# Kernel tuning notes

Measured on AMD Instinct MI355X. Metric: run time of the kernel, lower is better.

Reference implementation:

```python
import jax, jax.numpy as jnp
import numpy as np


def setup_inputs() -> dict:
    key = jax.random.key(0)
    ks = jax.random.split(key, 7)
    B, T, D, H, C = 256, 512, 128, 512, 10
    s_ih = 1.0 / np.sqrt(H)
    return {
        "X": jax.random.normal(ks[0], (B, T, D), dtype=jnp.float32),
        "W_ih": jax.random.normal(ks[1], (4 * H, D), dtype=jnp.float32) * s_ih,
        "W_hh": jax.random.normal(ks[2], (4 * H, H), dtype=jnp.float32) * s_ih,
        "b_ih": jax.random.normal(ks[3], (4 * H,), dtype=jnp.float32) * s_ih,
        "b_hh": jax.random.normal(ks[4], (4 * H,), dtype=jnp.float32) * s_ih,
        "W_lin": jax.random.normal(ks[5], (C, H), dtype=jnp.float32) * s_ih,
        "b_lin": jax.random.normal(ks[6], (C,), dtype=jnp.float32) * s_ih,
    }


def _lstm_mean_h(X, W_ih, W_hh, b_ih, b_hh):
    B, T, D = X.shape
    H = W_hh.shape[1]
    # Input projections for all timesteps at once: [T, B, 4H]
    x_proj = jnp.einsum("btd,kd->tbk", X, W_ih) + b_ih + b_hh

    def step(carry, xp):
        h, c = carry
        gates = xp + h @ W_hh.T  # [B, 4H]
        i, f, g, o = jnp.split(gates, 4, axis=-1)  # PyTorch i,f,g,o order
        i = jax.nn.sigmoid(i)
        f = jax.nn.sigmoid(f)
        g = jnp.tanh(g)
        o = jax.nn.sigmoid(o)
        c = f * c + i * g
        h = o * jnp.tanh(c)
        return (h, c), h

    h0 = jnp.zeros((B, H), dtype=X.dtype)
    (_, _), hs = jax.lax.scan(step, (h0, h0), x_proj)  # hs: [T, B, H]
    return jnp.mean(hs, axis=0)  # == sum(h_t)/T


def reference(X, W_ih, W_hh, b_ih, b_hh, W_lin, b_lin):
    states = _lstm_mean_h(X, W_ih, W_hh, b_ih, b_hh)  # [B, H]
    logits = states @ W_lin.T + b_lin  # [B, num_classes]
    return logits
```

## Files before the change

### kernel.cpp

```cpp
#include <hip/hip_runtime.h>
#include <stdint.h>


#define T_STEPS 512
#define BATCH   256
#define DIM     128
#define HID     512
#define NGRP    16
#define BT      16

typedef _Float16 half8 __attribute__((ext_vector_type(8)));
typedef _Float16 half4 __attribute__((ext_vector_type(4)));
typedef float    f32x4 __attribute__((ext_vector_type(4)));
typedef unsigned u32x4 __attribute__((ext_vector_type(4)));

#define SLOT_HALFS (BATCH * HID)
#define FLG_OFF    (2 * SLOT_HALFS * 2)
#define WS_NEEDED  (FLG_OFF + NGRP * 8 * 128)

__device__ __forceinline__ half8 cvt8(f32x4 a, f32x4 b) {
  half8 r;
  r[0]=(_Float16)a[0]; r[1]=(_Float16)a[1]; r[2]=(_Float16)a[2]; r[3]=(_Float16)a[3];
  r[4]=(_Float16)b[0]; r[5]=(_Float16)b[1]; r[6]=(_Float16)b[2]; r[7]=(_Float16)b[3];
  return r;
}
__device__ __forceinline__ half8 load8_cvt(const float* p) {
  const f32x4* q = (const f32x4*)p;
  return cvt8(q[0], q[1]);
}
__device__ __forceinline__ float fsig(float x) {
  return __builtin_amdgcn_rcpf(1.f + __expf(-x));
}
__device__ __forceinline__ float ftanh(float x) {
  return 1.f - 2.f * __builtin_amdgcn_rcpf(1.f + __expf(2.f * x));
}

union h4u { unsigned long long u; half4 h; };
union c16 { unsigned long long u2[2]; u32x4 v; };

__global__ __launch_bounds__(256, 1) void lstm_persistent(
    const float* __restrict__ X,   const float* __restrict__ Wih,
    const float* __restrict__ Whh, const float* __restrict__ bih,
    const float* __restrict__ bhh, const float* __restrict__ Wlin,
    float* __restrict__ out, _Float16* __restrict__ hbuf,
    unsigned* __restrict__ flg)
{
  __shared__ unsigned hsh[4096];

  const int tid  = threadIdx.x;
  const int w    = tid >> 6;
  const int lane = tid & 63;
  const int col  = lane & 15;
  const int q    = lane >> 4;
  const int bid  = blockIdx.x;
  const int g    = bid & 15;
  const int blk  = bid >> 4;
  const int J    = blk * 64 + w * 16;
  const int b_my = g * BT + col;

  half8 whh[16][4];
  half8 wih[4][4];
  #pragma unroll
  for (int kc = 0; kc < 16; ++kc)
    #pragma unroll
    for (int mt = 0; mt < 4; ++mt) {
      const int row = mt * HID + J + col;
      whh[kc][mt] = load8_cvt(Whh + (size_t)row * HID + kc * 32 + q * 8);
    }
  #pragma unroll
  for (int xc = 0; xc < 4; ++xc)
    #pragma unroll
    for (int mt = 0; mt < 4; ++mt) {
      const int row = mt * HID + J + col;
      wih[xc][mt] = load8_cvt(Wih + (size_t)row * DIM + xc * 32 + q * 8);
    }

  float bias[4][4], c_st[4], hsum[4];
  #pragma unroll
  for (int mt = 0; mt < 4; ++mt)
    #pragma unroll
    for (int r = 0; r < 4; ++r) {
      const int row = mt * HID + J + q * 4 + r;
      bias[mt][r] = bih[row] + bhh[row];
    }
  #pragma unroll
  for (int r = 0; r < 4; ++r) { c_st[r] = 0.f; hsum[r] = 0.f; }

  unsigned* gflg = flg + g * 8 * 32;
  const float* Xb = X + (size_t)b_my * T_STEPS * DIM;

  f32x4 xr0[8], xr1[8];
  #pragma unroll
  for (int xc = 0; xc < 4; ++xc) {
    const f32x4* p = (const f32x4*)(Xb + xc * 32 + q * 8);
    xr0[2 * xc] = p[0]; xr0[2 * xc + 1] = p[1];
  }
  f32x4 acc[4];
  #pragma unroll
  for (int mt = 0; mt < 4; ++mt) acc[mt] = (f32x4){0.f, 0.f, 0.f, 0.f};
  #pragma unroll
  for (int xc = 0; xc < 4; ++xc) {
    half8 xb = cvt8(xr0[2 * xc], xr0[2 * xc + 1]);
    #pragma unroll
    for (int mt = 0; mt < 4; ++mt)
      acc[mt] = __builtin_amdgcn_mfma_f32_16x16x32_f16(wih[xc][mt], xb, acc[mt], 0, 0, 0);
  }
  #pragma unroll
  for (int xc = 0; xc < 4; ++xc) {
    const f32x4* p1 = (const f32x4*)(Xb + (size_t)1 * DIM + xc * 32 + q * 8);
    const f32x4* p2 = (const f32x4*)(Xb + (size_t)2 * DIM + xc * 32 + q * 8);
    xr1[2 * xc] = p1[0]; xr1[2 * xc + 1] = p1[1];
    xr0[2 * xc] = p2[0]; xr0[2 * xc + 1] = p2[1];
  }

  for (int t = 0; t < T_STEPS; ++t) {
    if (t > 0) {
      {
        const int fl = lane & 7;
        for (;;) {
          unsigned v = __hip_atomic_load(gflg + fl * 32, __ATOMIC_RELAXED,
                                         __HIP_MEMORY_SCOPE_AGENT);
          if (fl == blk) v = 0xFFFFFFFFu;
          if (__all((int)(v >= (unsigned)t))) break;
        }
      }
      __builtin_amdgcn_sched_barrier(0);

      unsigned long long lo[4], hi[4];
      {
        const unsigned long long* base = (const unsigned long long*)
            (hbuf + (size_t)(t & 1) * SLOT_HALFS + (size_t)b_my * HID);
        #pragma unroll
        for (int i = 0; i < 4; ++i) {
          const int kc = w * 4 + i;
          lo[i] = __hip_atomic_load(base + kc * 8 + q * 2,     __ATOMIC_RELAXED, __HIP_MEMORY_SCOPE_AGENT);
          hi[i] = __hip_atomic_load(base + kc * 8 + q * 2 + 1, __ATOMIC_RELAXED, __HIP_MEMORY_SCOPE_AGENT);
        }
      }
      #pragma unroll
      for (int i = 0; i < 4; ++i) {
        const int kc = w * 4 + i;
        c16 u; u.u2[0] = lo[i]; u.u2[1] = hi[i];
        *(u32x4*)(hsh + kc * 256 + col * 16 + q * 4) = u.v;
      }
      __syncthreads();

      {
        const int tn = (t + 2 < T_STEPS) ? (t + 2) : (T_STEPS - 1);
        const float* xp = Xb + (size_t)tn * DIM + q * 8;
        f32x4* dst = (t & 1) ? xr1 : xr0;
        #pragma unroll
        for (int xc = 0; xc < 4; ++xc) {
          const f32x4* src = (const f32x4*)(xp + xc * 32);
          dst[2 * xc]     = src[0];
          dst[2 * xc + 1] = src[1];
        }
      }

      #pragma unroll
      for (int kc = 0; kc < 16; ++kc) {
        const half8 hb = *(const half8*)(hsh + kc * 256 + col * 16 + q * 4);
        #pragma unroll
        for (int mt = 0; mt < 4; ++mt)
          acc[mt] = __builtin_amdgcn_mfma_f32_16x16x32_f16(whh[kc][mt], hb, acc[mt], 0, 0, 0);
      }
    }

    h4u hv;
    #pragma unroll
    for (int r = 0; r < 4; ++r) {
      const float ig = fsig(acc[0][r] + bias[0][r]);
      const float fg = fsig(acc[1][r] + bias[1][r]);
      const float gg = ftanh(acc[2][r] + bias[2][r]);
      const float og = fsig(acc[3][r] + bias[3][r]);
      const float cc = fg * c_st[r] + ig * gg;
      c_st[r] = cc;
      const float h = og * ftanh(cc);
      hsum[r] += h;
      hv.h[r] = (_Float16)h;
    }

    if (t + 1 < T_STEPS) {
      unsigned long long* hw =
          (unsigned long long*)(hbuf + (size_t)((t + 1) & 1) * SLOT_HALFS
                                + (size_t)b_my * HID + J + q * 4);
      __hip_atomic_store(hw, hv.u, __ATOMIC_RELAXED, __HIP_MEMORY_SCOPE_AGENT);

      __syncthreads();
      if (tid == 0)
        __hip_atomic_store(gflg + blk * 32, (unsigned)(t + 1),
                           __ATOMIC_RELAXED, __HIP_MEMORY_SCOPE_AGENT);

      #pragma unroll
      for (int mt = 0; mt < 4; ++mt) acc[mt] = (f32x4){0.f, 0.f, 0.f, 0.f};
      const f32x4* xbuf = ((t + 1) & 1) ? xr1 : xr0;
      #pragma unroll
      for (int xc = 0; xc < 4; ++xc) {
        half8 xb = cvt8(xbuf[2 * xc], xbuf[2 * xc + 1]);
        #pragma unroll
        for (int mt = 0; mt < 4; ++mt)
          acc[mt] = __builtin_amdgcn_mfma_f32_16x16x32_f16(wih[xc][mt], xb, acc[mt], 0, 0, 0);
      }
    }
  }

  const float inv = 1.0f / (float)T_STEPS;
  float m[4];
  #pragma unroll
  for (int r = 0; r < 4; ++r) m[r] = hsum[r] * inv;
  #pragma unroll
  for (int cls = 0; cls < 10; ++cls) {
    f32x4 wl = *(const f32x4*)(Wlin + (size_t)cls * HID + J + q * 4);
    float p = m[0] * wl[0] + m[1] * wl[1] + m[2] * wl[2] + m[3] * wl[3];
    p += __shfl_xor(p, 16, 64);
    p += __shfl_xor(p, 32, 64);
    if (q == 0) atomicAdd(out + b_my * 10 + cls, p);
  }
}

__global__ void init_out(const float* __restrict__ blin, float* __restrict__ out) {
  const int i = blockIdx.x * blockDim.x + threadIdx.x;
  if (i < BATCH * 10) out[i] = blin[i % 10];
}

extern "C" void kernel_launch(void* const* d_in, const int* in_sizes, int n_in,
                              void* d_out, int out_size, void* d_ws, size_t ws_size,
                              hipStream_t stream) {
  const float* X    = (const float*)d_in[0];
  const float* Wih  = (const float*)d_in[1];
  const float* Whh  = (const float*)d_in[2];
  const float* bih  = (const float*)d_in[3];
  const float* bhh  = (const float*)d_in[4];
  const float* Wlin = (const float*)d_in[5];
  const float* blin = (const float*)d_in[6];
  float* out = (float*)d_out;

  if (ws_size < (size_t)WS_NEEDED) return;

  _Float16* hbuf = (_Float16*)d_ws;
  unsigned* flg  = (unsigned*)((char*)d_ws + FLG_OFF);

  hipMemsetAsync((char*)d_ws + FLG_OFF, 0, NGRP * 8 * 128, stream);
  init_out<<<10, 256, 0, stream>>>(blin, out);
  lstm_persistent<<<128, 256, 0, stream>>>(X, Wih, Whh, bih, bhh, Wlin, out,
                                           hbuf, flg);
}
```

Baseline: 2.832 ms.

## Replace per-block flag barrier with sentinel-valued data polling over a four-slot ring

Drops the per-group flag counters. Consumers now spin directly on the hidden-state data, which is held in a 4-deep ring buffer pre-filled with a sentinel bit pattern. Each producer rewrites its slot two steps ahead as a sentinel and publishes h without a block-wide syncthreads or a separate flag store. The first poll is issued speculatively right after publishing, and the shared-memory tile is double-buffered to avoid a second barrier. The aim is to remove the flag round-trip and barrier latency on the serial recurrence critical path. The cost is correctness risk: a real fp16 value could match the sentinel, and the scheme relies on relaxed-ordering assumptions. It also memsets a larger workspace on every call.

```diff
diff --git a/kernel.cpp b/kernel.cpp
--- a/kernel.cpp
+++ b/kernel.cpp
@@ -8,6 +8,7 @@
 #define HID     512
 #define NGRP    16
 #define BT      16
+#define RBUF    4
 
 typedef _Float16 half8 __attribute__((ext_vector_type(8)));
 typedef _Float16 half4 __attribute__((ext_vector_type(4)));
@@ -15,8 +16,9 @@
 typedef unsigned u32x4 __attribute__((ext_vector_type(4)));
 
 #define SLOT_HALFS (BATCH * HID)
-#define FLG_OFF    (2 * SLOT_HALFS * 2)
-#define WS_NEEDED  (FLG_OFF + NGRP * 8 * 128)
+#define SLOT_U64   (SLOT_HALFS / 4)
+#define WS_NEEDED  (RBUF * SLOT_HALFS * 2)
+#define SENT       0x7F7F7F7F7F7F7F7FULL
 
 __device__ __forceinline__ half8 cvt8(f32x4 a, f32x4 b) {
   half8 r;
@@ -42,10 +44,9 @@
     const float* __restrict__ X,   const float* __restrict__ Wih,
     const float* __restrict__ Whh, const float* __restrict__ bih,
     const float* __restrict__ bhh, const float* __restrict__ Wlin,
-    float* __restrict__ out, _Float16* __restrict__ hbuf,
-    unsigned* __restrict__ flg)
+    float* __restrict__ out, _Float16* __restrict__ hbuf)
 {
-  __shared__ unsigned hsh[4096];
+  __shared__ unsigned hsh[2][4096];
 
   const int tid  = threadIdx.x;
   const int w    = tid >> 6;
@@ -86,8 +87,10 @@
   #pragma unroll
   for (int r = 0; r < 4; ++r) { c_st[r] = 0.f; hsum[r] = 0.f; }
 
-  unsigned* gflg = flg + g * 8 * 32;
   const float* Xb = X + (size_t)b_my * T_STEPS * DIM;
+  unsigned long long* h64 = (unsigned long long*)hbuf;
+  const size_t pub_u64 = ((size_t)b_my * HID + J + q * 4) >> 2;
+  const size_t con_u64 = (((size_t)b_my * HID) >> 2) + q * 2;
 
   f32x4 xr0[8], xr1[8];
   #pragma unroll
@@ -113,56 +116,46 @@
     xr0[2 * xc] = p2[0]; xr0[2 * xc + 1] = p2[1];
   }
 
+  unsigned long long lo[4], hi[4];
+  #pragma unroll
+  for (int i = 0; i < 4; ++i) { lo[i] = SENT; hi[i] = SENT; }
+
   for (int t = 0; t < T_STEPS; ++t) {
+    __hip_atomic_store(h64 + (size_t)((t + 2) & 3) * SLOT_U64 + pub_u64,
+                       (unsigned long long)SENT, __ATOMIC_RELAXED,
+                       __HIP_MEMORY_SCOPE_AGENT);
+
     if (t > 0) {
-      {
-        const int fl = lane & 7;
-        for (;;) {
-          unsigned v = __hip_atomic_load(gflg + fl * 32, __ATOMIC_RELAXED,
-                                         __HIP_MEMORY_SCOPE_AGENT);
-          if (fl == blk) v = 0xFFFFFFFFu;
-          if (__all((int)(v >= (unsigned)t))) break;
-        }
-      }
-      __builtin_amdgcn_sched_barrier(0);
-
-      unsigned long long lo[4], hi[4];
-      {
-        const unsigned long long* base = (const unsigned long long*)
-            (hbuf + (size_t)(t & 1) * SLOT_HALFS + (size_t)b_my * HID);
+      const unsigned long long* hp = h64 + (size_t)(t & 3) * SLOT_U64 + con_u64;
+      for (;;) {
+        int ok = 1;
+        #pragma unroll
+        for (int i = 0; i < 4; ++i)
+          ok &= (int)(lo[i] != SENT) & (int)(hi[i] != SENT);
+        if (__all(ok)) break;
         #pragma unroll
         for (int i = 0; i < 4; ++i) {
           const int kc = w * 4 + i;
-          lo[i] = __hip_atomic_load(base + kc * 8 + q * 2,     __ATOMIC_RELAXED, __HIP_MEMORY_SCOPE_AGENT);
-          hi[i] = __hip_atomic_load(base + kc * 8 + q * 2 + 1, __ATOMIC_RELAXED, __HIP_MEMORY_SCOPE_AGENT);
+          lo[i] = __hip_atomic_load(hp + kc * 8,     __ATOMIC_RELAXED, __HIP_MEMORY_SCOPE_AGENT);
+          hi[i] = __hip_atomic_load(hp + kc * 8 + 1, __ATOMIC_RELAXED, __HIP_MEMORY_SCOPE_AGENT);
         }
       }
+      __builtin_amdgcn_sched_barrier(0);
+
       #pragma unroll
       for (int i = 0; i < 4; ++i) {
         const int kc = w * 4 + i;
         c16 u; u.u2[0] = lo[i]; u.u2[1] = hi[i];
-        *(u32x4*)(hsh + kc * 256 + col * 16 + q * 4) = u.v;
+        *(u32x4*)(&hsh[t & 1][kc * 256 + q * 64 + col * 4]) = u.v;
       }
       __syncthreads();
 
-      {
-        const int tn = (t + 2 < T_STEPS) ? (t + 2) : (T_STEPS - 1);
-        const float* xp = Xb + (size_t)tn * DIM + q * 8;
-        f32x4* dst = (t & 1) ? xr1 : xr0;
-        #pragma unroll
-        for (int xc = 0; xc < 4; ++xc) {
-          const f32x4* src = (const f32x4*)(xp + xc * 32);
-          dst[2 * xc]     = src[0];
-          dst[2 * xc + 1] = src[1];
-        }
-      }
-
       #pragma unroll
       for (int kc = 0; kc < 16; ++kc) {
-        const half8 hb = *(const half8*)(hsh + kc * 256 + col * 16 + q * 4);
+        const half8 hbv = *(const half8*)(&hsh[t & 1][kc * 256 + q * 64 + col * 4]);
         #pragma unroll
         for (int mt = 0; mt < 4; ++mt)
-          acc[mt] = __builtin_amdgcn_mfma_f32_16x16x32_f16(whh[kc][mt], hb, acc[mt], 0, 0, 0);
+          acc[mt] = __builtin_amdgcn_mfma_f32_16x16x32_f16(whh[kc][mt], hbv, acc[mt], 0, 0, 0);
       }
     }
 
@@ -181,15 +174,33 @@
     }
 
     if (t + 1 < T_STEPS) {
-      unsigned long long* hw =
-          (unsigned long long*)(hbuf + (size_t)((t + 1) & 1) * SLOT_HALFS
-                                + (size_t)b_my * HID + J + q * 4);
-      __hip_atomic_store(hw, hv.u, __ATOMIC_RELAXED, __HIP_MEMORY_SCOPE_AGENT);
-
-      __syncthreads();
-      if (tid == 0)
-        __hip_atomic_store(gflg + blk * 32, (unsigned)(t + 1),
-                           __ATOMIC_RELAXED, __HIP_MEMORY_SCOPE_AGENT);
+      asm volatile("s_waitcnt vmcnt(0)" ::: "memory");
+
+      __hip_atomic_store(h64 + (size_t)((t + 1) & 3) * SLOT_U64 + pub_u64,
+                         hv.u, __ATOMIC_RELAXED, __HIP_MEMORY_SCOPE_AGENT);
+
+      {
+        const unsigned long long* hp2 =
+            h64 + (size_t)((t + 1) & 3) * SLOT_U64 + con_u64;
+        #pragma unroll
+        for (int i = 0; i < 4; ++i) {
+          const int kc = w * 4 + i;
+          lo[i] = __hip_atomic_load(hp2 + kc * 8,     __ATOMIC_RELAXED, __HIP_MEMORY_SCOPE_AGENT);
+          hi[i] = __hip_atomic_load(hp2 + kc * 8 + 1, __ATOMIC_RELAXED, __HIP_MEMORY_SCOPE_AGENT);
+        }
+      }
+
+      {
+        const int tn = (t + 2 < T_STEPS) ? (t + 2) : (T_STEPS - 1);
+        const float* xp = Xb + (size_t)tn * DIM + q * 8;
+        f32x4* dst = (t & 1) ? xr1 : xr0;
+        #pragma unroll
+        for (int xc = 0; xc < 4; ++xc) {
+          const f32x4* src = (const f32x4*)(xp + xc * 32);
+          dst[2 * xc]     = src[0];
+          dst[2 * xc + 1] = src[1];
+        }
+      }
 
       #pragma unroll
       for (int mt = 0; mt < 4; ++mt) acc[mt] = (f32x4){0.f, 0.f, 0.f, 0.f};
@@ -238,10 +249,9 @@
   if (ws_size < (size_t)WS_NEEDED) return;
 
   _Float16* hbuf = (_Float16*)d_ws;
-  unsigned* flg  = (unsigned*)((char*)d_ws + FLG_OFF);
-
-  hipMemsetAsync((char*)d_ws + FLG_OFF, 0, NGRP * 8 * 128, stream);
+
+  hipMemsetAsync(d_ws, 0x7F, WS_NEEDED, stream);
   init_out<<<10, 256, 0, stream>>>(blin, out);
   lstm_persistent<<<128, 256, 0, stream>>>(X, Wih, Whh, bih, bhh, Wlin, out,
-                                           hbuf, flg);
-}
+                                           hbuf);
+}
```

Result: slower. 3.735 ms (+31.9%).

## Replace per-block step flags with per-wave flags and ring-buffer hidden state

Applied to the files above, without the earlier changes.

Each wave now publishes its slice of h and raises its own readiness flag after waiting only for its own stores. This removes the block-wide barrier before signalling. Consumers poll just the 8 producer waves whose columns they read. To stay safe without that barrier, h moves to a 4-slot global ring and the LDS staging buffer is double-buffered, so faster waves cannot overwrite data still being read. The X prefetch for step t+2 moves after the publish so it stays off the critical path, at the cost of more flag memory and polling traffic.

```diff
diff --git a/kernel.cpp b/kernel.cpp
--- a/kernel.cpp
+++ b/kernel.cpp
@@ -8,6 +8,7 @@
 #define HID     512
 #define NGRP    16
 #define BT      16
+#define RBUF    4
 
 typedef _Float16 half8 __attribute__((ext_vector_type(8)));
 typedef _Float16 half4 __attribute__((ext_vector_type(4)));
@@ -15,8 +16,9 @@
 typedef unsigned u32x4 __attribute__((ext_vector_type(4)));
 
 #define SLOT_HALFS (BATCH * HID)
-#define FLG_OFF    (2 * SLOT_HALFS * 2)
-#define WS_NEEDED  (FLG_OFF + NGRP * 8 * 128)
+#define SLOT_U64   (SLOT_HALFS / 4)
+#define FLG_OFF    (RBUF * SLOT_HALFS * 2)
+#define WS_NEEDED  (FLG_OFF + NGRP * 32 * 128)
 
 __device__ __forceinline__ half8 cvt8(f32x4 a, f32x4 b) {
   half8 r;
@@ -45,7 +47,7 @@
     float* __restrict__ out, _Float16* __restrict__ hbuf,
     unsigned* __restrict__ flg)
 {
-  __shared__ unsigned hsh[4096];
+  __shared__ unsigned hsh[2][4096];
 
   const int tid  = threadIdx.x;
   const int w    = tid >> 6;
@@ -56,6 +58,7 @@
   const int g    = bid & 15;
   const int blk  = bid >> 4;
   const int J    = blk * 64 + w * 16;
+  const int wid  = blk * 4 + w;
   const int b_my = g * BT + col;
 
   half8 whh[16][4];
@@ -86,8 +89,15 @@
   #pragma unroll
   for (int r = 0; r < 4; ++r) { c_st[r] = 0.f; hsum[r] = 0.f; }
 
-  unsigned* gflg = flg + g * 8 * 32;
+  unsigned* gflg = flg + (size_t)g * 32 * 32;
   const float* Xb = X + (size_t)b_my * T_STEPS * DIM;
+  unsigned long long* h64 = (unsigned long long*)hbuf;
+  const size_t pub_u64 = ((size_t)b_my * HID + J + q * 4) >> 2;
+  const size_t con_u64 = ((size_t)b_my * HID) >> 2;
+
+  const int  pw   = 8 * w + (lane & 7);
+  const bool self = (pw == wid);
+  unsigned* pollp = gflg + (size_t)pw * 32;
 
   f32x4 xr0[8], xr1[8];
   #pragma unroll
@@ -115,21 +125,18 @@
 
   for (int t = 0; t < T_STEPS; ++t) {
     if (t > 0) {
-      {
-        const int fl = lane & 7;
-        for (;;) {
-          unsigned v = __hip_atomic_load(gflg + fl * 32, __ATOMIC_RELAXED,
-                                         __HIP_MEMORY_SCOPE_AGENT);
-          if (fl == blk) v = 0xFFFFFFFFu;
-          if (__all((int)(v >= (unsigned)t))) break;
-        }
+      for (;;) {
+        unsigned v = __hip_atomic_load(pollp, __ATOMIC_RELAXED,
+                                       __HIP_MEMORY_SCOPE_AGENT);
+        if (self) v = 0xFFFFFFFFu;
+        if (__all((int)(v >= (unsigned)t))) break;
       }
       __builtin_amdgcn_sched_barrier(0);
 
       unsigned long long lo[4], hi[4];
       {
-        const unsigned long long* base = (const unsigned long long*)
-            (hbuf + (size_t)(t & 1) * SLOT_HALFS + (size_t)b_my * HID);
+        const unsigned long long* base =
+            h64 + (size_t)(t & 3) * SLOT_U64 + con_u64;
         #pragma unroll
         for (int i = 0; i < 4; ++i) {
           const int kc = w * 4 + i;
@@ -141,28 +148,16 @@
       for (int i = 0; i < 4; ++i) {
         const int kc = w * 4 + i;
         c16 u; u.u2[0] = lo[i]; u.u2[1] = hi[i];
-        *(u32x4*)(hsh + kc * 256 + col * 16 + q * 4) = u.v;
+        *(u32x4*)(&hsh[t & 1][kc * 256 + q * 64 + col * 4]) = u.v;
       }
       __syncthreads();
 
-      {
-        const int tn = (t + 2 < T_STEPS) ? (t + 2) : (T_STEPS - 1);
-        const float* xp = Xb + (size_t)tn * DIM + q * 8;
-        f32x4* dst = (t & 1) ? xr1 : xr0;
-        #pragma unroll
-        for (int xc = 0; xc < 4; ++xc) {
-          const f32x4* src = (const f32x4*)(xp + xc * 32);
-          dst[2 * xc]     = src[0];
-          dst[2 * xc + 1] = src[1];
-        }
-      }
-
       #pragma unroll
       for (int kc = 0; kc < 16; ++kc) {
-        const half8 hb = *(const half8*)(hsh + kc * 256 + col * 16 + q * 4);
+        const half8 hbv = *(const half8*)(&hsh[t & 1][kc * 256 + q * 64 + col * 4]);
         #pragma unroll
         for (int mt = 0; mt < 4; ++mt)
-          acc[mt] = __builtin_amdgcn_mfma_f32_16x16x32_f16(whh[kc][mt], hb, acc[mt], 0, 0, 0);
+          acc[mt] = __builtin_amdgcn_mfma_f32_16x16x32_f16(whh[kc][mt], hbv, acc[mt], 0, 0, 0);
       }
     }
 
@@ -181,15 +176,25 @@
     }
 
     if (t + 1 < T_STEPS) {
-      unsigned long long* hw =
-          (unsigned long long*)(hbuf + (size_t)((t + 1) & 1) * SLOT_HALFS
-                                + (size_t)b_my * HID + J + q * 4);
-      __hip_atomic_store(hw, hv.u, __ATOMIC_RELAXED, __HIP_MEMORY_SCOPE_AGENT);
-
-      __syncthreads();
-      if (tid == 0)
-        __hip_atomic_store(gflg + blk * 32, (unsigned)(t + 1),
+      __hip_atomic_store(h64 + (size_t)((t + 1) & 3) * SLOT_U64 + pub_u64,
+                         hv.u, __ATOMIC_RELAXED, __HIP_MEMORY_SCOPE_AGENT);
+
+      asm volatile("s_waitcnt vmcnt(0)" ::: "memory");
+      if (lane == 0)
+        __hip_atomic_store(gflg + (size_t)wid * 32, (unsigned)(t + 1),
                            __ATOMIC_RELAXED, __HIP_MEMORY_SCOPE_AGENT);
+
+      {
+        const int tn = (t + 2 < T_STEPS) ? (t + 2) : (T_STEPS - 1);
+        const float* xp = Xb + (size_t)tn * DIM + q * 8;
+        f32x4* dst = (t & 1) ? xr1 : xr0;
+        #pragma unroll
+        for (int xc = 0; xc < 4; ++xc) {
+          const f32x4* src = (const f32x4*)(xp + xc * 32);
+          dst[2 * xc]     = src[0];
+          dst[2 * xc + 1] = src[1];
+        }
+      }
 
       #pragma unroll
       for (int mt = 0; mt < 4; ++mt) acc[mt] = (f32x4){0.f, 0.f, 0.f, 0.f};
@@ -240,7 +245,7 @@
   _Float16* hbuf = (_Float16*)d_ws;
   unsigned* flg  = (unsigned*)((char*)d_ws + FLG_OFF);
 
-  hipMemsetAsync((char*)d_ws + FLG_OFF, 0, NGRP * 8 * 128, stream);
+  hipMemsetAsync((char*)d_ws + FLG_OFF, 0, NGRP * 32 * 128, stream);
   init_out<<<10, 256, 0, stream>>>(blin, out);
   lstm_persistent<<<128, 256, 0, stream>>>(X, Wih, Whh, bih, bhh, Wlin, out,
                                            hbuf, flg);
```

New measurement: 2.884 ms. Within noise of the previous version (+1.8%).
